# Optimization experiments

Hardware: AMD Instinct MI355X
Metric: run time of the kernel (lower is better)

The kernel has to match this reference:

```python
import jax, jax.numpy as jnp
import numpy as np

NEG_SLOPE = 0.2

def gat_conv(x, src, dst, W, a_src, a_dst, bias, num_nodes, heads, out_ch, concat):
    # x: [N, Fin]; W: [Fin, heads*out_ch]; a_src/a_dst: [heads, out_ch]
    h = (x @ W).reshape(num_nodes, heads, out_ch)            # [N,H,C]
    alpha_s = jnp.einsum('nhc,hc->nh', h, a_src)             # [N,H]
    alpha_d = jnp.einsum('nhc,hc->nh', h, a_dst)             # [N,H]
    e = alpha_s[src] + alpha_d[dst]                          # [E,H]
    e = jnp.where(e > 0, e, NEG_SLOPE * e)                   # LeakyReLU
    # segment softmax over incoming edges per destination node
    m = jax.ops.segment_max(e, dst, num_segments=num_nodes)  # [N,H]
    m = jnp.where(jnp.isfinite(m), m, 0.0)
    ee = jnp.exp(e - m[dst])                                 # [E,H]
    s = jax.ops.segment_sum(ee, dst, num_segments=num_nodes) # [N,H]
    alpha = ee / (s[dst] + 1e-16)                            # [E,H]
    out = jax.ops.segment_sum(h[src] * alpha[:, :, None], dst,
                              num_segments=num_nodes)        # [N,H,C]
    if concat:
        out = out.reshape(num_nodes, heads * out_ch)
    else:
        out = out.mean(axis=1)
    return out + bias


def setup_inputs() -> dict:
    key = jax.random.key(0)
    ks = jax.random.split(key, 10)
    N, E = 50000, 800000
    EMB, HID, HEADS, REPR = 128, 128, 8, 64
    C1 = HID // HEADS  # 16
    x = jax.random.normal(ks[0], (N, EMB), dtype=jnp.float32)
    edge_index = jax.random.randint(ks[1], (2, E), 0, N, dtype=jnp.int32)
    sc = 1.0 / np.sqrt(EMB)
    W1 = jax.random.normal(ks[2], (EMB, HEADS * C1), dtype=jnp.float32) * sc
    a1_src = jax.random.normal(ks[3], (HEADS, C1), dtype=jnp.float32) * 0.1
    a1_dst = jax.random.normal(ks[4], (HEADS, C1), dtype=jnp.float32) * 0.1
    b1 = jnp.zeros((HID,), dtype=jnp.float32)
    sc2 = 1.0 / np.sqrt(HID)
    W2 = jax.random.normal(ks[5], (HID, REPR), dtype=jnp.float32) * sc2
    a2_src = jax.random.normal(ks[6], (1, REPR), dtype=jnp.float32) * 0.1
    a2_dst = jax.random.normal(ks[7], (1, REPR), dtype=jnp.float32) * 0.1
    b2 = jnp.zeros((REPR,), dtype=jnp.float32)
    return {"x": x, "edge_index": edge_index,
            "W1": W1, "a1_src": a1_src, "a1_dst": a1_dst, "b1": b1,
            "W2": W2, "a2_src": a2_src, "a2_dst": a2_dst, "b2": b2}


def reference(x, edge_index, W1, a1_src, a1_dst, b1, W2, a2_src, a2_dst, b2):
    N = x.shape[0]
    # PyG GATConv adds self-loops by default
    loops = jnp.arange(N, dtype=edge_index.dtype)
    src = jnp.concatenate([edge_index[0], loops])
    dst = jnp.concatenate([edge_index[1], loops])
    # eval mode: F.dropout(p=0.6) is identity
    h = gat_conv(x, src, dst, W1, a1_src, a1_dst, b1, N,
                 heads=8, out_ch=16, concat=True)
    h = jax.nn.elu(h)
    out = gat_conv(h, src, dst, W2, a2_src, a2_dst, b2, N,
                   heads=1, out_ch=64, concat=True)
    return out
```

## Files before the change

### kernel.cpp

```cpp
#include <hip/hip_runtime.h>
#include <hip/hip_fp16.h>
#include <math.h>


typedef _Float16 f16x8 __attribute__((ext_vector_type(8)));
typedef float f32x4 __attribute__((ext_vector_type(4)));

#define NCHUNK 32
#define MAXBDIV 8192

__device__ __forceinline__ float leaky_exp(float e) {
    e = (e > 0.f) ? e : 0.2f * e;
    return __expf(e);
}

__device__ __forceinline__ void acc16(float w, float4 hv0, float4 hv1,
                                      float* __restrict__ acc) {
    const __half2* p0 = (const __half2*)&hv0;
    const __half2* p1 = (const __half2*)&hv1;
#pragma unroll
    for (int k = 0; k < 4; k++) {
        float2 f = __half22float2(p0[k]);
        acc[2 * k] += w * f.x;
        acc[2 * k + 1] += w * f.y;
    }
#pragma unroll
    for (int k = 0; k < 4; k++) {
        float2 f = __half22float2(p1[k]);
        acc[8 + 2 * k] += w * f.x;
        acc[8 + 2 * k + 1] += w * f.y;
    }
}

__device__ __forceinline__ void acc8(float w, float4 hv,
                                     float* __restrict__ acc) {
    const __half2* hp = (const __half2*)&hv;
#pragma unroll
    for (int k = 0; k < 4; k++) {
        float2 f = __half22float2(hp[k]);
        acc[2 * k] += w * f.x;
        acc[2 * k + 1] += w * f.y;
    }
}

__global__ __launch_bounds__(256) void augw_kernel(const float* __restrict__ W1,
                                                   const float* __restrict__ a1s,
                                                   const float* __restrict__ a1d,
                                                   const float* __restrict__ W2,
                                                   const float* __restrict__ a2s,
                                                   const float* __restrict__ a2d,
                                                   _Float16* __restrict__ W1t,
                                                   _Float16* __restrict__ W2t) {
    int t = threadIdx.x;
    if (blockIdx.x == 0) {
        for (int i = t; i < 144 * 128; i += 256) {
            int c = i >> 7, k = i & 127;
            float v;
            if (c < 128) {
                v = W1[k * 128 + c];
            } else if (c < 136) {
                int h = c - 128; v = 0.f;
#pragma unroll
                for (int j = 0; j < 16; j++) v += W1[k * 128 + h * 16 + j] * a1s[h * 16 + j];
            } else {
                int h = c - 136; v = 0.f;
#pragma unroll
                for (int j = 0; j < 16; j++) v += W1[k * 128 + h * 16 + j] * a1d[h * 16 + j];
            }
            W1t[c * 128 + k] = (_Float16)v;
        }
    } else {
        for (int i = t; i < 80 * 128; i += 256) {
            int c = i >> 7, k = i & 127;
            float v = 0.f;
            if (c < 64) {
                v = W2[k * 64 + c];
            } else if (c == 64) {
                for (int j = 0; j < 64; j++) v += W2[k * 64 + j] * a2s[j];
            } else if (c == 65) {
                for (int j = 0; j < 64; j++) v += W2[k * 64 + j] * a2d[j];
            }
            W2t[c * 128 + k] = (_Float16)v;
        }
    }
}

__global__ __launch_bounds__(256) void gemm1_bucket_kernel(
        const float* __restrict__ x, const _Float16* __restrict__ W1t,
        __half* __restrict__ h1, float* __restrict__ als,
        float* __restrict__ ald, int N, int gridG1,
        const int* __restrict__ src, const int* __restrict__ dst, int E,
        int* __restrict__ bucketCnt, unsigned* __restrict__ pairs) {
    __shared__ _Float16 Xs[64 * 136];
    int t = threadIdx.x;
    if ((int)blockIdx.x >= gridG1) {
        int* lcnt = (int*)Xs;
        int* lbase = lcnt + 8;
        if (t < 8) lcnt[t] = 0;
        __syncthreads();
        int bid = blockIdx.x - gridG1;
        int bdiv = (N + 7) >> 3;
        int i0 = (bid * 256 + t) * 4;
        int s_[4], d_[4], bk[4], rk[4];
        int nv = 0;
        if (i0 + 3 < E) {
            int4 d4 = *(const int4*)(dst + i0);
            int4 s4 = *(const int4*)(src + i0);
            s_[0] = s4.x; s_[1] = s4.y; s_[2] = s4.z; s_[3] = s4.w;
            d_[0] = d4.x; d_[1] = d4.y; d_[2] = d4.z; d_[3] = d4.w;
            nv = 4;
        } else {
            for (int k = i0; k < E && nv < 4; k++) {
                s_[nv] = src[k]; d_[nv] = dst[k]; nv++;
            }
        }
        int lane = t & 63;
        unsigned long long below = (lane == 0) ? 0ULL : (~0ULL >> (64 - lane));
#pragma unroll
        for (int u = 0; u < 4; u++) {
            bool v = (u < nv);
            int d = v ? d_[u] : 0;
            int b = d / bdiv;
            unsigned long long m0 = __ballot(b & 1);
            unsigned long long m1 = __ballot(b & 2);
            unsigned long long m2 = __ballot(b & 4);
            unsigned long long vm = __ballot(v);
            unsigned long long me = ((b & 1) ? m0 : ~m0) & ((b & 2) ? m1 : ~m1) &
                                    ((b & 4) ? m2 : ~m2) & vm;
            int leader = __ffsll((unsigned long long)me) - 1;
            int ldr = (leader < 0) ? 0 : leader;
            int cnt = __popcll(me);
            int rank = __popcll(me & below);
            int base = 0;
            if (v && lane == leader) base = atomicAdd(&lcnt[b], cnt);
            base = __shfl(base, ldr);
            bk[u] = b;
            rk[u] = base + rank;
        }
        __syncthreads();
        if (t < 8) lbase[t] = atomicAdd(&bucketCnt[t * 16], lcnt[t]);
        __syncthreads();
#pragma unroll 4
        for (int k = 0; k < nv; k++) {
            unsigned dlocal = (unsigned)(d_[k] - bk[k] * ((N + 7) >> 3));
            pairs[(size_t)bk[k] * E + lbase[bk[k]] + rk[k]] =
                (dlocal << 16) | (unsigned)s_[k];
        }
        return;
    }
    int row0 = blockIdx.x * 64;
    for (int i = t; i < 2048; i += 256) {
        int r = i >> 5, c4 = i & 31;
        int gr = row0 + r;
        float4 v = make_float4(0.f, 0.f, 0.f, 0.f);
        if (gr < N) v = *(const float4*)(x + (size_t)gr * 128 + c4 * 4);
        _Float16* dp = Xs + r * 136 + c4 * 4;
        dp[0] = (_Float16)v.x; dp[1] = (_Float16)v.y;
        dp[2] = (_Float16)v.z; dp[3] = (_Float16)v.w;
    }
    __syncthreads();
    int w = t >> 6, L = t & 63, m = L & 15, quad = L >> 4;
    f32x4 acc[9];
#pragma unroll
    for (int f = 0; f < 9; f++) acc[f] = (f32x4){0.f, 0.f, 0.f, 0.f};
    const _Float16* Arow = Xs + (w * 16 + m) * 136 + quad * 8;
    const _Float16* Brow = W1t + m * 128 + quad * 8;
#pragma unroll
    for (int kt = 0; kt < 4; kt++) {
        f16x8 a = *(const f16x8*)(Arow + kt * 32);
#pragma unroll
        for (int f = 0; f < 9; f++) {
            f16x8 b = *(const f16x8*)(Brow + f * 2048 + kt * 32);
            acc[f] = __builtin_amdgcn_mfma_f32_16x16x32_f16(a, b, acc[f], 0, 0, 0);
        }
    }
    int nbase = row0 + w * 16 + quad * 4;
#pragma unroll
    for (int r = 0; r < 4; r++) {
        int n = nbase + r;
        if (n < N) {
            __half* hrow = h1 + (size_t)n * 128 + m;
#pragma unroll
            for (int f = 0; f < 8; f++) hrow[f * 16] = __float2half(acc[f][r]);
            float v = acc[8][r];
            if (m < 8) als[n * 8 + m] = v;
            else ald[n * 8 + (m - 8)] = v;
        }
    }
}

__global__ __launch_bounds__(256) void subhist_kernel(
        const int* __restrict__ bucketCnt, const unsigned* __restrict__ pairs,
        int E, int N, int* __restrict__ subcnt) {
    __shared__ int hist[MAXBDIV];
    int t = threadIdx.x;
    int b = blockIdx.x & 7;
    int j = blockIdx.x >> 3;
    int bdiv = (N + 7) >> 3;
    for (int i = t; i < bdiv; i += 256) hist[i] = 0;
    __syncthreads();
    int cnt = bucketCnt[b * 16];
    int chunk = (cnt + NCHUNK - 1) / NCHUNK;
    int lo = j * chunk;
    int hi = min(lo + chunk, cnt);
    const unsigned* plist = pairs + (size_t)b * E;
    for (int i = lo + t; i < hi; i += 256) {
        atomicAdd(&hist[plist[i] >> 16], 1);
    }
    __syncthreads();
    int* out = subcnt + (size_t)(b * NCHUNK + j) * bdiv;
    for (int i = t; i < bdiv; i += 256) out[i] = hist[i];
}

__global__ __launch_bounds__(256) void scan1_kernel(const int* __restrict__ subcnt,
                                                    int N,
                                                    int* __restrict__ rowstart,
                                                    int* __restrict__ blocksum) {
    __shared__ int tmp[256];
    int t = threadIdx.x;
    int i = blockIdx.x * 256 + t;
    int bdiv = (N + 7) >> 3;
    int v = 0;
    if (i < N) {
        int b = i / bdiv;
        int local = i - b * bdiv;
        const int* sc = subcnt + (size_t)b * NCHUNK * bdiv + local;
#pragma unroll
        for (int j = 0; j < NCHUNK; j++) v += sc[(size_t)j * bdiv];
    }
    tmp[t] = v;
    __syncthreads();
    for (int off = 1; off < 256; off <<= 1) {
        int x = (t >= off) ? tmp[t - off] : 0;
        __syncthreads();
        tmp[t] += x;
        __syncthreads();
    }
    if (i < N) rowstart[i] = tmp[t] - v;
    if (t == 255) blocksum[blockIdx.x] = tmp[t];
}

__global__ __launch_bounds__(256) void scan23_kernel(int* __restrict__ rowstart,
                                                     const int* __restrict__ blocksum,
                                                     int nb,
                                                     int* __restrict__ subcnt,
                                                     int N, int E) {
    __shared__ int sdata[256];
    int t = threadIdx.x;
    int bx = blockIdx.x;
    sdata[t] = (t < nb && t < bx) ? blocksum[t] : 0;
    __syncthreads();
#pragma unroll
    for (int off = 128; off > 0; off >>= 1) {
        if (t < off) sdata[t] += sdata[t + off];
        __syncthreads();
    }
    int offset = sdata[0];
    int i = bx * 256 + t;
    int bdiv = (N + 7) >> 3;
    if (i < N) {
        int v = rowstart[i] + offset;
        rowstart[i] = v;
        int b = i / bdiv;
        int local = i - b * bdiv;
        int* sc = subcnt + (size_t)b * NCHUNK * bdiv + local;
        int c = v;
#pragma unroll
        for (int j = 0; j < NCHUNK; j++) {
            int cj = sc[(size_t)j * bdiv];
            sc[(size_t)j * bdiv] = c;
            c += cj;
        }
    } else if (i == N) {
        rowstart[N] = E;
    }
}

__global__ __launch_bounds__(256) void scatter_kernel(
        const int* __restrict__ bucketCnt, const unsigned* __restrict__ pairs,
        int E, int N, const int* __restrict__ subcnt, int* __restrict__ esrc) {
    __shared__ int lcur[MAXBDIV];
    int t = threadIdx.x;
    int b = blockIdx.x & 7;
    int j = blockIdx.x >> 3;
    int bdiv = (N + 7) >> 3;
    const int* base = subcnt + (size_t)(b * NCHUNK + j) * bdiv;
    for (int i = t; i < bdiv; i += 256) lcur[i] = base[i];
    __syncthreads();
    int cnt = bucketCnt[b * 16];
    int chunk = (cnt + NCHUNK - 1) / NCHUNK;
    int lo = j * chunk;
    int hi = min(lo + chunk, cnt);
    const unsigned* plist = pairs + (size_t)b * E;
    for (int i = lo + t; i < hi; i += 256) {
        unsigned p = plist[i];
        int pos = atomicAdd(&lcur[p >> 16], 1);
        esrc[pos] = (int)(p & 0xFFFFu);
    }
}

__global__ __launch_bounds__(256) void agg1_gemm2_kernel(
        const __half* __restrict__ h1, const float* __restrict__ als,
        const float* __restrict__ ald, const int* __restrict__ rowstart,
        const int* __restrict__ esrc, const float* __restrict__ b1,
        const _Float16* __restrict__ W2t, __half* __restrict__ h2,
        float* __restrict__ al2s, float* __restrict__ al2d, int N) {
    __shared__ _Float16 actS[32 * 136];
    int t = threadIdx.x;
    int lane = t & 63;
    int grp = lane >> 3;
    int q = lane & 7;
    int bdiv = (N + 7) >> 3;
    int lrow = (t >> 6) * 8 + grp;
    int ln = (blockIdx.x >> 3) * 32 + lrow;
    int n = (blockIdx.x & 7) * bdiv + ln;
    bool valid = (ln < bdiv) && (n < N);
    const float4* h1v = (const float4*)h1;
    float acc[16];
#pragma unroll
    for (int k = 0; k < 16; k++) acc[k] = 0.f;
    float wsum = 0.f;
    int beg = 0, end = 0;
    float adv = 0.f;
    if (valid) {
        adv = ald[n * 8 + q];
        float wself = leaky_exp(als[n * 8 + q] + adv);
        wsum = wself;
        acc16(wself, h1v[(size_t)n * 16 + 2 * q], h1v[(size_t)n * 16 + 2 * q + 1], acc);
        beg = rowstart[n];
        end = rowstart[n + 1];
    }
    int j = beg;
    for (; j + 4 <= end; j += 4) {
        int s0 = esrc[j], s1 = esrc[j + 1], s2 = esrc[j + 2], s3 = esrc[j + 3];
        float4 a0 = h1v[(size_t)s0 * 16 + 2 * q], b0 = h1v[(size_t)s0 * 16 + 2 * q + 1];
        float4 a1 = h1v[(size_t)s1 * 16 + 2 * q], b1v = h1v[(size_t)s1 * 16 + 2 * q + 1];
        float4 a2 = h1v[(size_t)s2 * 16 + 2 * q], b2 = h1v[(size_t)s2 * 16 + 2 * q + 1];
        float4 a3 = h1v[(size_t)s3 * 16 + 2 * q], b3 = h1v[(size_t)s3 * 16 + 2 * q + 1];
        float e0 = als[s0 * 8 + q], e1 = als[s1 * 8 + q];
        float e2 = als[s2 * 8 + q], e3 = als[s3 * 8 + q];
        float w0 = leaky_exp(e0 + adv), w1 = leaky_exp(e1 + adv);
        float w2 = leaky_exp(e2 + adv), w3 = leaky_exp(e3 + adv);
        wsum += (w0 + w1) + (w2 + w3);
        acc16(w0, a0, b0, acc);
        acc16(w1, a1, b1v, acc);
        acc16(w2, a2, b2, acc);
        acc16(w3, a3, b3, acc);
    }
    for (; j < end; j++) {
        int s = esrc[j];
        float w = leaky_exp(als[s * 8 + q] + adv);
        wsum += w;
        acc16(w, h1v[(size_t)s * 16 + 2 * q], h1v[(size_t)s * 16 + 2 * q + 1], acc);
    }
    __align__(16) __half2 po[8];
    if (valid) {
        float inv = 1.f / (wsum + 1e-16f);
        const float* bf = b1 + q * 16;
#pragma unroll
        for (int k = 0; k < 8; k++) {
            float o0 = acc[2 * k] * inv + bf[2 * k];
            float o1 = acc[2 * k + 1] * inv + bf[2 * k + 1];
            o0 = (o0 > 0.f) ? o0 : (__expf(o0) - 1.f);
            o1 = (o1 > 0.f) ? o1 : (__expf(o1) - 1.f);
            po[k] = __floats2half2_rn(o0, o1);
        }
    } else {
#pragma unroll
        for (int k = 0; k < 8; k++) po[k] = __floats2half2_rn(0.f, 0.f);
    }
    *(float4*)(actS + lrow * 136 + q * 16) = ((float4*)po)[0];
    *(float4*)(actS + lrow * 136 + q * 16 + 8) = ((float4*)po)[1];
    __syncthreads();
    int w4 = t >> 6;
    int m = lane & 15, quad = lane >> 4;
    int rt = w4 & 1;
    int ctbase = (w4 < 2) ? 0 : 1;
    f32x4 acc2[3];
#pragma unroll
    for (int f = 0; f < 3; f++) acc2[f] = (f32x4){0.f, 0.f, 0.f, 0.f};
    const _Float16* Arow2 = actS + (rt * 16 + m) * 136 + quad * 8;
    const _Float16* Brow2 = W2t + m * 128 + quad * 8;
#pragma unroll
    for (int kt = 0; kt < 4; kt++) {
        f16x8 a = *(const f16x8*)(Arow2 + kt * 32);
#pragma unroll
        for (int f = 0; f < 3; f++) {
            int ctf = ctbase + 2 * f;
            if (ctf < 5) {
                f16x8 bb = *(const f16x8*)(Brow2 + ctf * 2048 + kt * 32);
                acc2[f] = __builtin_amdgcn_mfma_f32_16x16x32_f16(a, bb, acc2[f], 0, 0, 0);
            }
        }
    }
    int secbase = (blockIdx.x & 7) * bdiv;
    int lnbase = (blockIdx.x >> 3) * 32 + rt * 16 + quad * 4;
#pragma unroll
    for (int r = 0; r < 4; r++) {
        int ln2 = lnbase + r;
        int n2 = secbase + ln2;
        if (ln2 < bdiv && n2 < N) {
#pragma unroll
            for (int f = 0; f < 3; f++) {
                int ctf = ctbase + 2 * f;
                if (ctf < 4) {
                    h2[(size_t)n2 * 64 + ctf * 16 + m] = __float2half(acc2[f][r]);
                } else if (ctf == 4) {
                    if (m == 0) al2s[n2] = acc2[f][r];
                    else if (m == 1) al2d[n2] = acc2[f][r];
                }
            }
        }
    }
}

__global__ __launch_bounds__(256) void agg2_kernel(const __half* __restrict__ h2,
                                                   const float* __restrict__ al2s,
                                                   const float* __restrict__ al2d,
                                                   const int* __restrict__ rowstart,
                                                   const int* __restrict__ esrc,
                                                   const float* __restrict__ b2,
                                                   float* __restrict__ out, int N) {
    int t = threadIdx.x;
    int lane = t & 63;
    int grp = lane >> 3;
    int q = lane & 7;
    int bdiv = (N + 7) >> 3;
    int ln = (blockIdx.x >> 3) * 32 + (t >> 6) * 8 + grp;
    if (ln >= bdiv) return;
    int n = (blockIdx.x & 7) * bdiv + ln;
    if (n >= N) return;
    const float4* h2v = (const float4*)h2;
    float adv = al2d[n];
    float acc[8];
#pragma unroll
    for (int k = 0; k < 8; k++) acc[k] = 0.f;
    float wsum = 0.f;
    {
        float w = leaky_exp(al2s[n] + adv);
        wsum += w;
        acc8(w, h2v[(size_t)n * 8 + q], acc);
    }
    int beg = rowstart[n], end = rowstart[n + 1];
    int j = beg;
    for (; j + 4 <= end; j += 4) {
        int s0 = esrc[j], s1 = esrc[j + 1], s2 = esrc[j + 2], s3 = esrc[j + 3];
        float4 a0 = h2v[(size_t)s0 * 8 + q];
        float4 a1 = h2v[(size_t)s1 * 8 + q];
        float4 a2 = h2v[(size_t)s2 * 8 + q];
        float4 a3 = h2v[(size_t)s3 * 8 + q];
        float e0 = al2s[s0], e1 = al2s[s1], e2 = al2s[s2], e3 = al2s[s3];
        float w0 = leaky_exp(e0 + adv), w1 = leaky_exp(e1 + adv);
        float w2 = leaky_exp(e2 + adv), w3 = leaky_exp(e3 + adv);
        wsum += (w0 + w1) + (w2 + w3);
        acc8(w0, a0, acc);
        acc8(w1, a1, acc);
        acc8(w2, a2, acc);
        acc8(w3, a3, acc);
    }
    for (; j < end; j++) {
        int s = esrc[j];
        float w = leaky_exp(al2s[s] + adv);
        wsum += w;
        acc8(w, h2v[(size_t)s * 8 + q], acc);
    }
    float inv = 1.f / (wsum + 1e-16f);
    const float* bf = b2 + q * 8;
    float4* ov = (float4*)(out + (size_t)n * 64 + q * 8);
    ov[0] = make_float4(acc[0] * inv + bf[0], acc[1] * inv + bf[1],
                        acc[2] * inv + bf[2], acc[3] * inv + bf[3]);
    ov[1] = make_float4(acc[4] * inv + bf[4], acc[5] * inv + bf[5],
                        acc[6] * inv + bf[6], acc[7] * inv + bf[7]);
}

extern "C" void kernel_launch(void* const* d_in, const int* in_sizes, int n_in,
                              void* d_out, int out_size, void* d_ws, size_t ws_size,
                              hipStream_t stream) {
    (void)n_in; (void)out_size; (void)ws_size;
    const float* x   = (const float*)d_in[0];
    const int*   ei  = (const int*)d_in[1];
    const float* W1  = (const float*)d_in[2];
    const float* a1s = (const float*)d_in[3];
    const float* a1d = (const float*)d_in[4];
    const float* b1  = (const float*)d_in[5];
    const float* W2  = (const float*)d_in[6];
    const float* a2s = (const float*)d_in[7];
    const float* a2d = (const float*)d_in[8];
    const float* b2  = (const float*)d_in[9];
    float* out = (float*)d_out;

    const int N = in_sizes[0] / 128;
    const int E = in_sizes[1] / 2;
    const int* src = ei;
    const int* dst = ei + E;
    const int bdiv = (N + 7) / 8;

    char* wp = (char*)d_ws;
    auto alloc = [&](size_t bytes) -> void* {
        void* p = (void*)wp;
        wp += (bytes + 255) & ~(size_t)255;
        return p;
    };
    __half* h1   = (__half*)alloc((size_t)N * 128 * 2);
    __half* h2   = (__half*)alloc((size_t)N * 64 * 2 + 64 * 256);
    float* al1s = (float*)alloc((size_t)N * 8 * 4);
    float* al1d = (float*)alloc((size_t)N * 8 * 4);
    float* al2s = (float*)alloc((size_t)N * 4);
    float* al2d = (float*)alloc((size_t)N * 4);
    int* bucketCnt = (int*)alloc(8 * 16 * 4);
    int* subcnt   = (int*)alloc((size_t)8 * NCHUNK * bdiv * 4);
    int* rowstart = (int*)alloc((size_t)(N + 1) * 4);
    int* esrc     = (int*)alloc((size_t)E * 4);
    unsigned* pairs = (unsigned*)alloc((size_t)8 * E * 4);
    int* blocksum = (int*)alloc(256 * 4);
    _Float16* W1t = (_Float16*)alloc(144 * 128 * 2);
    _Float16* W2t = (_Float16*)alloc(80 * 128 * 2);

    const int nbScan = (N + 255) / 256;
    const int gridH  = (E + 1023) / 1024;
    const int gridG1 = (N + 63) / 64;
    const int gridAggN = 8 * ((bdiv + 31) / 32);
    const int gridSort = 8 * NCHUNK;

    hipMemsetAsync(bucketCnt, 0, 8 * 16 * 4, stream);

    augw_kernel<<<2, 256, 0, stream>>>(W1, a1s, a1d, W2, a2s, a2d, W1t, W2t);
    gemm1_bucket_kernel<<<gridG1 + gridH, 256, 0, stream>>>(
        x, W1t, h1, al1s, al1d, N, gridG1, src, dst, E, bucketCnt, pairs);
    subhist_kernel<<<gridSort, 256, 0, stream>>>(bucketCnt, pairs, E, N, subcnt);
    scan1_kernel<<<nbScan, 256, 0, stream>>>(subcnt, N, rowstart, blocksum);
    scan23_kernel<<<(N + 256) / 256, 256, 0, stream>>>(rowstart, blocksum, nbScan,
                                                       subcnt, N, E);
    scatter_kernel<<<gridSort, 256, 0, stream>>>(bucketCnt, pairs, E, N, subcnt, esrc);

    agg1_gemm2_kernel<<<gridAggN, 256, 0, stream>>>(h1, al1s, al1d, rowstart, esrc,
                                                    b1, W2t, h2, al2s, al2d, N);
    agg2_kernel<<<gridAggN, 256, 0, stream>>>(h2, al2s, al2d, rowstart, esrc, b2, out, N);
}
```

Before: 220.8 us.

## Redistribute gemm1 tiles across sort kernels to overlap with bucketing work

Edge bucketing now runs together with the weight augmentation kernel. The first GEMM's row tiles are split in half, and each half is co-scheduled inside the subhistogram and scatter kernels. The aim is to fill idle CUs during the small-grid sort phases and so shorten the critical path. In exchange, the GEMM blocks now use a 32KB LDS allocation, which may lower occupancy for the GEMM tiles.

```diff
diff --git a/kernel.cpp b/kernel.cpp
--- a/kernel.cpp
+++ b/kernel.cpp
@@ -43,14 +43,59 @@
     }
 }
 
-__global__ __launch_bounds__(256) void augw_kernel(const float* __restrict__ W1,
-                                                   const float* __restrict__ a1s,
-                                                   const float* __restrict__ a1d,
-                                                   const float* __restrict__ W2,
-                                                   const float* __restrict__ a2s,
-                                                   const float* __restrict__ a2d,
-                                                   _Float16* __restrict__ W1t,
-                                                   _Float16* __restrict__ W2t) {
+__device__ __forceinline__ void gemm1_tile(
+        const float* __restrict__ x, const _Float16* __restrict__ W1t,
+        __half* __restrict__ h1, float* __restrict__ als,
+        float* __restrict__ ald, int N, int row0, _Float16* Xs, int t) {
+    for (int i = t; i < 2048; i += 256) {
+        int r = i >> 5, c4 = i & 31;
+        int gr = row0 + r;
+        float4 v = make_float4(0.f, 0.f, 0.f, 0.f);
+        if (gr < N) v = *(const float4*)(x + (size_t)gr * 128 + c4 * 4);
+        _Float16* dp = Xs + r * 136 + c4 * 4;
+        dp[0] = (_Float16)v.x; dp[1] = (_Float16)v.y;
+        dp[2] = (_Float16)v.z; dp[3] = (_Float16)v.w;
+    }
+    __syncthreads();
+    int w = t >> 6, L = t & 63, m = L & 15, quad = L >> 4;
+    f32x4 acc[9];
+#pragma unroll
+    for (int f = 0; f < 9; f++) acc[f] = (f32x4){0.f, 0.f, 0.f, 0.f};
+    const _Float16* Arow = Xs + (w * 16 + m) * 136 + quad * 8;
+    const _Float16* Brow = W1t + m * 128 + quad * 8;
+#pragma unroll
+    for (int kt = 0; kt < 4; kt++) {
+        f16x8 a = *(const f16x8*)(Arow + kt * 32);
+#pragma unroll
+        for (int f = 0; f < 9; f++) {
+            f16x8 b = *(const f16x8*)(Brow + f * 2048 + kt * 32);
+            acc[f] = __builtin_amdgcn_mfma_f32_16x16x32_f16(a, b, acc[f], 0, 0, 0);
+        }
+    }
+    int nbase = row0 + w * 16 + quad * 4;
+#pragma unroll
+    for (int r = 0; r < 4; r++) {
+        int n = nbase + r;
+        if (n < N) {
+            __half* hrow = h1 + (size_t)n * 128 + m;
+#pragma unroll
+            for (int f = 0; f < 8; f++) hrow[f * 16] = __float2half(acc[f][r]);
+            float v = acc[8][r];
+            if (m < 8) als[n * 8 + m] = v;
+            else ald[n * 8 + (m - 8)] = v;
+        }
+    }
+}
+
+__global__ __launch_bounds__(256) void augw_bucket_kernel(
+        const float* __restrict__ W1, const float* __restrict__ a1s,
+        const float* __restrict__ a1d, const float* __restrict__ W2,
+        const float* __restrict__ a2s, const float* __restrict__ a2d,
+        _Float16* __restrict__ W1t, _Float16* __restrict__ W2t,
+        const int* __restrict__ src, const int* __restrict__ dst,
+        int E, int N, int* __restrict__ bucketCnt, unsigned* __restrict__ pairs) {
+    __shared__ int lcnt[8];
+    __shared__ int lbase[8];
     int t = threadIdx.x;
     if (blockIdx.x == 0) {
         for (int i = t; i < 144 * 128; i += 256) {
@@ -69,7 +114,9 @@
             }
             W1t[c * 128 + k] = (_Float16)v;
         }
-    } else {
+        return;
+    }
+    if (blockIdx.x == 1) {
         for (int i = t; i < 80 * 128; i += 256) {
             int c = i >> 7, k = i & 127;
             float v = 0.f;
@@ -82,122 +129,78 @@
             }
             W2t[c * 128 + k] = (_Float16)v;
         }
-    }
-}
-
-__global__ __launch_bounds__(256) void gemm1_bucket_kernel(
+        return;
+    }
+    if (t < 8) lcnt[t] = 0;
+    __syncthreads();
+    int bid = blockIdx.x - 2;
+    int bdiv = (N + 7) >> 3;
+    int i0 = (bid * 256 + t) * 4;
+    int s_[4], d_[4], bk[4], rk[4];
+    int nv = 0;
+    if (i0 + 3 < E) {
+        int4 d4 = *(const int4*)(dst + i0);
+        int4 s4 = *(const int4*)(src + i0);
+        s_[0] = s4.x; s_[1] = s4.y; s_[2] = s4.z; s_[3] = s4.w;
+        d_[0] = d4.x; d_[1] = d4.y; d_[2] = d4.z; d_[3] = d4.w;
+        nv = 4;
+    } else {
+        for (int k = i0; k < E && nv < 4; k++) {
+            s_[nv] = src[k]; d_[nv] = dst[k]; nv++;
+        }
+    }
+    int lane = t & 63;
+    unsigned long long below = (lane == 0) ? 0ULL : (~0ULL >> (64 - lane));
+#pragma unroll
+    for (int u = 0; u < 4; u++) {
+        bool v = (u < nv);
+        int d = v ? d_[u] : 0;
+        int b = d / bdiv;
+        unsigned long long m0 = __ballot(b & 1);
+        unsigned long long m1 = __ballot(b & 2);
+        unsigned long long m2 = __ballot(b & 4);
+        unsigned long long vm = __ballot(v);
+        unsigned long long me = ((b & 1) ? m0 : ~m0) & ((b & 2) ? m1 : ~m1) &
+                                ((b & 4) ? m2 : ~m2) & vm;
+        int leader = __ffsll((unsigned long long)me) - 1;
+        int ldr = (leader < 0) ? 0 : leader;
+        int cnt = __popcll(me);
+        int rank = __popcll(me & below);
+        int base = 0;
+        if (v && lane == leader) base = atomicAdd(&lcnt[b], cnt);
+        base = __shfl(base, ldr);
+        bk[u] = b;
+        rk[u] = base + rank;
+    }
+    __syncthreads();
+    if (t < 8) lbase[t] = atomicAdd(&bucketCnt[t * 16], lcnt[t]);
+    __syncthreads();
+#pragma unroll 4
+    for (int k = 0; k < nv; k++) {
+        unsigned dlocal = (unsigned)(d_[k] - bk[k] * ((N + 7) >> 3));
+        pairs[(size_t)bk[k] * E + lbase[bk[k]] + rk[k]] =
+            (dlocal << 16) | (unsigned)s_[k];
+    }
+}
+
+__global__ __launch_bounds__(256) void gemm1_subhist_kernel(
         const float* __restrict__ x, const _Float16* __restrict__ W1t,
         __half* __restrict__ h1, float* __restrict__ als,
-        float* __restrict__ ald, int N, int gridG1,
-        const int* __restrict__ src, const int* __restrict__ dst, int E,
-        int* __restrict__ bucketCnt, unsigned* __restrict__ pairs) {
-    __shared__ _Float16 Xs[64 * 136];
-    int t = threadIdx.x;
-    if ((int)blockIdx.x >= gridG1) {
-        int* lcnt = (int*)Xs;
-        int* lbase = lcnt + 8;
-        if (t < 8) lcnt[t] = 0;
-        __syncthreads();
-        int bid = blockIdx.x - gridG1;
-        int bdiv = (N + 7) >> 3;
-        int i0 = (bid * 256 + t) * 4;
-        int s_[4], d_[4], bk[4], rk[4];
-        int nv = 0;
-        if (i0 + 3 < E) {
-            int4 d4 = *(const int4*)(dst + i0);
-            int4 s4 = *(const int4*)(src + i0);
-            s_[0] = s4.x; s_[1] = s4.y; s_[2] = s4.z; s_[3] = s4.w;
-            d_[0] = d4.x; d_[1] = d4.y; d_[2] = d4.z; d_[3] = d4.w;
-            nv = 4;
-        } else {
-            for (int k = i0; k < E && nv < 4; k++) {
-                s_[nv] = src[k]; d_[nv] = dst[k]; nv++;
-            }
-        }
-        int lane = t & 63;
-        unsigned long long below = (lane == 0) ? 0ULL : (~0ULL >> (64 - lane));
-#pragma unroll
-        for (int u = 0; u < 4; u++) {
-            bool v = (u < nv);
-            int d = v ? d_[u] : 0;
-            int b = d / bdiv;
-            unsigned long long m0 = __ballot(b & 1);
-            unsigned long long m1 = __ballot(b & 2);
-            unsigned long long m2 = __ballot(b & 4);
-            unsigned long long vm = __ballot(v);
-            unsigned long long me = ((b & 1) ? m0 : ~m0) & ((b & 2) ? m1 : ~m1) &
-                                    ((b & 4) ? m2 : ~m2) & vm;
-            int leader = __ffsll((unsigned long long)me) - 1;
-            int ldr = (leader < 0) ? 0 : leader;
-            int cnt = __popcll(me);
-            int rank = __popcll(me & below);
-            int base = 0;
-            if (v && lane == leader) base = atomicAdd(&lcnt[b], cnt);
-            base = __shfl(base, ldr);
-            bk[u] = b;
-            rk[u] = base + rank;
-        }
-        __syncthreads();
-        if (t < 8) lbase[t] = atomicAdd(&bucketCnt[t * 16], lcnt[t]);
-        __syncthreads();
-#pragma unroll 4
-        for (int k = 0; k < nv; k++) {
-            unsigned dlocal = (unsigned)(d_[k] - bk[k] * ((N + 7) >> 3));
-            pairs[(size_t)bk[k] * E + lbase[bk[k]] + rk[k]] =
-                (dlocal << 16) | (unsigned)s_[k];
-        }
+        float* __restrict__ ald, int N, int rowOff, int nGemm,
+        const int* __restrict__ bucketCnt, const unsigned* __restrict__ pairs,
+        int E, int* __restrict__ subcnt) {
+    __shared__ int ldsbuf[MAXBDIV];
+    int t = threadIdx.x;
+    if ((int)blockIdx.x < nGemm) {
+        gemm1_tile(x, W1t, h1, als, ald, N, (rowOff + blockIdx.x) * 64,
+                   (_Float16*)ldsbuf, t);
         return;
     }
-    int row0 = blockIdx.x * 64;
-    for (int i = t; i < 2048; i += 256) {
-        int r = i >> 5, c4 = i & 31;
-        int gr = row0 + r;
-        float4 v = make_float4(0.f, 0.f, 0.f, 0.f);
-        if (gr < N) v = *(const float4*)(x + (size_t)gr * 128 + c4 * 4);
-        _Float16* dp = Xs + r * 136 + c4 * 4;
-        dp[0] = (_Float16)v.x; dp[1] = (_Float16)v.y;
-        dp[2] = (_Float16)v.z; dp[3] = (_Float16)v.w;
-    }
-    __syncthreads();
-    int w = t >> 6, L = t & 63, m = L & 15, quad = L >> 4;
-    f32x4 acc[9];
-#pragma unroll
-    for (int f = 0; f < 9; f++) acc[f] = (f32x4){0.f, 0.f, 0.f, 0.f};
-    const _Float16* Arow = Xs + (w * 16 + m) * 136 + quad * 8;
-    const _Float16* Brow = W1t + m * 128 + quad * 8;
-#pragma unroll
-    for (int kt = 0; kt < 4; kt++) {
-        f16x8 a = *(const f16x8*)(Arow + kt * 32);
-#pragma unroll
-        for (int f = 0; f < 9; f++) {
-            f16x8 b = *(const f16x8*)(Brow + f * 2048 + kt * 32);
-            acc[f] = __builtin_amdgcn_mfma_f32_16x16x32_f16(a, b, acc[f], 0, 0, 0);
-        }
-    }
-    int nbase = row0 + w * 16 + quad * 4;
-#pragma unroll
-    for (int r = 0; r < 4; r++) {
-        int n = nbase + r;
-        if (n < N) {
-            __half* hrow = h1 + (size_t)n * 128 + m;
-#pragma unroll
-            for (int f = 0; f < 8; f++) hrow[f * 16] = __float2half(acc[f][r]);
-            float v = acc[8][r];
-            if (m < 8) als[n * 8 + m] = v;
-            else ald[n * 8 + (m - 8)] = v;
-        }
-    }
-}
-
-__global__ __launch_bounds__(256) void subhist_kernel(
-        const int* __restrict__ bucketCnt, const unsigned* __restrict__ pairs,
-        int E, int N, int* __restrict__ subcnt) {
-    __shared__ int hist[MAXBDIV];
-    int t = threadIdx.x;
-    int b = blockIdx.x & 7;
-    int j = blockIdx.x >> 3;
-    int bdiv = (N + 7) >> 3;
-    for (int i = t; i < bdiv; i += 256) hist[i] = 0;
+    int sbid = blockIdx.x - nGemm;
+    int b = sbid & 7;
+    int j = sbid >> 3;
+    int bdiv = (N + 7) >> 3;
+    for (int i = t; i < bdiv; i += 256) ldsbuf[i] = 0;
     __syncthreads();
     int cnt = bucketCnt[b * 16];
     int chunk = (cnt + NCHUNK - 1) / NCHUNK;
@@ -205,11 +208,11 @@
     int hi = min(lo + chunk, cnt);
     const unsigned* plist = pairs + (size_t)b * E;
     for (int i = lo + t; i < hi; i += 256) {
-        atomicAdd(&hist[plist[i] >> 16], 1);
+        atomicAdd(&ldsbuf[plist[i] >> 16], 1);
     }
     __syncthreads();
     int* out = subcnt + (size_t)(b * NCHUNK + j) * bdiv;
-    for (int i = t; i < bdiv; i += 256) out[i] = hist[i];
+    for (int i = t; i < bdiv; i += 256) out[i] = ldsbuf[i];
 }
 
 __global__ __launch_bounds__(256) void scan1_kernel(const int* __restrict__ subcnt,
@@ -276,16 +279,25 @@
     }
 }
 
-__global__ __launch_bounds__(256) void scatter_kernel(
+__global__ __launch_bounds__(256) void gemm1_scatter_kernel(
+        const float* __restrict__ x, const _Float16* __restrict__ W1t,
+        __half* __restrict__ h1, float* __restrict__ als,
+        float* __restrict__ ald, int N, int rowOff, int nGemm,
         const int* __restrict__ bucketCnt, const unsigned* __restrict__ pairs,
-        int E, int N, const int* __restrict__ subcnt, int* __restrict__ esrc) {
-    __shared__ int lcur[MAXBDIV];
-    int t = threadIdx.x;
-    int b = blockIdx.x & 7;
-    int j = blockIdx.x >> 3;
+        int E, const int* __restrict__ subcnt, int* __restrict__ esrc) {
+    __shared__ int ldsbuf[MAXBDIV];
+    int t = threadIdx.x;
+    if ((int)blockIdx.x < nGemm) {
+        gemm1_tile(x, W1t, h1, als, ald, N, (rowOff + blockIdx.x) * 64,
+                   (_Float16*)ldsbuf, t);
+        return;
+    }
+    int sbid = blockIdx.x - nGemm;
+    int b = sbid & 7;
+    int j = sbid >> 3;
     int bdiv = (N + 7) >> 3;
     const int* base = subcnt + (size_t)(b * NCHUNK + j) * bdiv;
-    for (int i = t; i < bdiv; i += 256) lcur[i] = base[i];
+    for (int i = t; i < bdiv; i += 256) ldsbuf[i] = base[i];
     __syncthreads();
     int cnt = bucketCnt[b * 16];
     int chunk = (cnt + NCHUNK - 1) / NCHUNK;
@@ -294,7 +306,7 @@
     const unsigned* plist = pairs + (size_t)b * E;
     for (int i = lo + t; i < hi; i += 256) {
         unsigned p = plist[i];
-        int pos = atomicAdd(&lcur[p >> 16], 1);
+        int pos = atomicAdd(&ldsbuf[p >> 16], 1);
         esrc[pos] = (int)(p & 0xFFFFu);
     }
 }
@@ -519,19 +531,23 @@
     const int nbScan = (N + 255) / 256;
     const int gridH  = (E + 1023) / 1024;
     const int gridG1 = (N + 63) / 64;
+    const int g1A = gridG1 / 2;
+    const int g1B = gridG1 - g1A;
     const int gridAggN = 8 * ((bdiv + 31) / 32);
     const int gridSort = 8 * NCHUNK;
 
     hipMemsetAsync(bucketCnt, 0, 8 * 16 * 4, stream);
 
-    augw_kernel<<<2, 256, 0, stream>>>(W1, a1s, a1d, W2, a2s, a2d, W1t, W2t);
-    gemm1_bucket_kernel<<<gridG1 + gridH, 256, 0, stream>>>(
-        x, W1t, h1, al1s, al1d, N, gridG1, src, dst, E, bucketCnt, pairs);
-    subhist_kernel<<<gridSort, 256, 0, stream>>>(bucketCnt, pairs, E, N, subcnt);
+    augw_bucket_kernel<<<2 + gridH, 256, 0, stream>>>(
+        W1, a1s, a1d, W2, a2s, a2d, W1t, W2t, src, dst, E, N, bucketCnt, pairs);
+    gemm1_subhist_kernel<<<g1A + gridSort, 256, 0, stream>>>(
+        x, W1t, h1, al1s, al1d, N, 0, g1A, bucketCnt, pairs, E, subcnt);
     scan1_kernel<<<nbScan, 256, 0, stream>>>(subcnt, N, rowstart, blocksum);
     scan23_kernel<<<(N + 256) / 256, 256, 0, stream>>>(rowstart, blocksum, nbScan,
                                                        subcnt, N, E);
-    scatter_kernel<<<gridSort, 256, 0, stream>>>(bucketCnt, pairs, E, N, subcnt, esrc);
+    gemm1_scatter_kernel<<<g1B + gridSort, 256, 0, stream>>>(
+        x, W1t, h1, al1s, al1d, N, g1A, g1B, bucketCnt, pairs, E,
+        subcnt, esrc);
 
     agg1_gemm2_kernel<<<gridAggN, 256, 0, stream>>>(h1, al1s, al1d, rowstart, esrc,
                                                     b1, W2t, h2, al2s, al2d, N);
```

Measured after the change: 224.2 us. No clear change (+1.5%).
